# Optimization experiments

Measured on AMD Instinct MI355X. Metric: run time of the kernel, lower is better.

## Reference

```python
import jax, jax.numpy as jnp
import numpy as np

N = 50000
E = 800000
C = 96


def _mlp(x, W1, b1, W2, b2, out_act=None):
    # 2-layer MLP: Linear -> SiLU -> Linear -> (optional output activation)
    h = jax.nn.silu(x @ W1 + b1)
    y = h @ W2 + b2
    return y if out_act is None else out_act(y)


def setup_inputs() -> dict:
    key = jax.random.key(0)
    ks = jax.random.split(key, 16)
    s = 1.0 / np.sqrt(C)
    inp = {
        "node_feats": jax.random.normal(ks[0], (N, C), jnp.float32),
        "coordinates": jax.random.normal(ks[1], (N, 3), jnp.float32),
        "m_ji": jax.random.normal(ks[2], (E, C), jnp.float32),
        "edge_indices": jax.random.randint(ks[3], (2, E), 0, N, jnp.int64),
        # phi_n: 2C -> C -> C
        "Wn1": jax.random.normal(ks[4], (2 * C, C), jnp.float32) * s,
        "bn1": jnp.zeros((C,), jnp.float32),
        "Wn2": jax.random.normal(ks[5], (C, C), jnp.float32) * s,
        "bn2": jnp.zeros((C,), jnp.float32),
        # attention: C -> C -> 1, Sigmoid output
        "Wa1": jax.random.normal(ks[6], (C, C), jnp.float32) * s,
        "ba1": jnp.zeros((C,), jnp.float32),
        "Wa2": jax.random.normal(ks[7], (C, 1), jnp.float32) * s,
        "ba2": jnp.zeros((1,), jnp.float32),
        # phi_x: C -> C -> 1, no output activation
        "Wx1": jax.random.normal(ks[8], (C, C), jnp.float32) * s,
        "bx1": jnp.zeros((C,), jnp.float32),
        "Wx2": jax.random.normal(ks[9], (C, 1), jnp.float32) * s,
        "bx2": jnp.zeros((1,), jnp.float32),
    }
    return inp


def reference(node_feats, coordinates, m_ji, edge_indices,
              Wn1, bn1, Wn2, bn2, Wa1, ba1, Wa2, ba2, Wx1, bx1, Wx2, bx2):
    num_nodes = node_feats.shape[0]
    receiver = edge_indices[0]
    sender = edge_indices[1]

    # edge attention: [E, 1]
    attention_ji = _mlp(m_ji, Wa1, ba1, Wa2, ba2, out_act=jax.nn.sigmoid)

    # attention-weighted scatter-sum of messages into nodes: [N, C]
    m_i = jax.ops.segment_sum(m_ji * attention_ji, receiver, num_segments=num_nodes)

    # residual node update
    node_feats = _mlp(jnp.concatenate([node_feats, m_i], axis=-1), Wn1, bn1, Wn2, bn2) + node_feats

    # coordinate update (non-periodic: cell=None)
    r_ji = coordinates[sender] - coordinates[receiver]            # [E, 3]
    abs_r_ji = jnp.linalg.norm(r_ji, axis=-1, keepdims=True)       # [E, 1]
    delta_coords_ji = r_ji / (abs_r_ji + 1.0) * _mlp(m_ji, Wx1, bx1, Wx2, bx2)
    delta_coords_i = jax.ops.segment_sum(delta_coords_ji, receiver, num_segments=num_nodes)
    coordinates = coordinates + delta_coords_i

    return node_feats, coordinates, attention_ji
```

## Files before the change

### kernel.cpp

```cpp
#include <hip/hip_runtime.h>
#include <cstddef>

#define TC 96
#define BM 64
#define NT 256
#define AST 100
#define XST 204
#define HST 100

__device__ __forceinline__ float fsigmoid(float x) {
    return 1.0f / (1.0f + __expf(-x));
}

__global__ __launch_bounds__(NT, 4)
void edge_kernel(const float* __restrict__ m_ji,
                 const int*   __restrict__ edge_idx,
                 const float* __restrict__ coords,
                 const float* __restrict__ Wa1, const float* __restrict__ ba1,
                 const float* __restrict__ Wa2, const float* __restrict__ ba2,
                 const float* __restrict__ Wx1, const float* __restrict__ bx1,
                 const float* __restrict__ Wx2, const float* __restrict__ bx2,
                 float* __restrict__ m_acc,
                 float* __restrict__ out_coords,
                 float* __restrict__ out_att,
                 int E)
{
    __shared__ float A[BM][AST];
    __shared__ float s_att[BM];
    __shared__ float s_phx[BM];
    __shared__ int   s_recv[BM];
    __shared__ int   s_send[BM];

    const int tid  = threadIdx.x;
    const int e0   = blockIdx.x * BM;
    const int rows = (E - e0 < BM) ? (E - e0) : BM;

    if (tid < BM) {
        const int e = (tid < rows) ? (e0 + tid) : (E - 1);
        s_recv[tid] = edge_idx[e];
        s_send[tid] = edge_idx[E + e];
    }
    for (int i4 = tid; i4 < BM * (TC / 4); i4 += NT) {
        const int r  = i4 / (TC / 4);
        const int c4 = i4 % (TC / 4);
        const int er = (r < rows) ? (e0 + r) : (E - 1);
        const float4 v = *reinterpret_cast<const float4*>(m_ji + (size_t)er * TC + c4 * 4);
        *reinterpret_cast<float4*>(&A[r][c4 * 4]) = v;
    }
    __syncthreads();

    const int tx = tid & 15;
    const int ty = tid >> 4;
    const int r0 = ty * 4;
    const bool isAtt = (tx < 8);
    const float* __restrict__ Bp = isAtt ? (Wa1 + tx * 12) : (Wx1 + (tx - 8) * 12);

    float acc[4][12];
    #pragma unroll
    for (int q = 0; q < 4; ++q) {
        #pragma unroll
        for (int j = 0; j < 12; ++j) acc[q][j] = 0.0f;
    }

    #pragma unroll 2
    for (int k = 0; k < TC; ++k) {
        const float4 b0 = *reinterpret_cast<const float4*>(Bp + (size_t)k * TC + 0);
        const float4 b1 = *reinterpret_cast<const float4*>(Bp + (size_t)k * TC + 4);
        const float4 b2 = *reinterpret_cast<const float4*>(Bp + (size_t)k * TC + 8);
        const float bv[12] = {b0.x, b0.y, b0.z, b0.w,
                              b1.x, b1.y, b1.z, b1.w,
                              b2.x, b2.y, b2.z, b2.w};
        const float a0 = A[r0 + 0][k];
        const float a1 = A[r0 + 1][k];
        const float a2 = A[r0 + 2][k];
        const float a3 = A[r0 + 3][k];
        #pragma unroll
        for (int j = 0; j < 12; ++j) {
            acc[0][j] = fmaf(a0, bv[j], acc[0][j]);
            acc[1][j] = fmaf(a1, bv[j], acc[1][j]);
            acc[2][j] = fmaf(a2, bv[j], acc[2][j]);
            acc[3][j] = fmaf(a3, bv[j], acc[3][j]);
        }
    }

    const float* __restrict__ b1p = isAtt ? (ba1 + tx * 12) : (bx1 + (tx - 8) * 12);
    const float* __restrict__ w2p = isAtt ? (Wa2 + tx * 12) : (Wx2 + (tx - 8) * 12);
    float b1v[12], w2v[12];
    #pragma unroll
    for (int j = 0; j < 12; ++j) { b1v[j] = b1p[j]; w2v[j] = w2p[j]; }

    float red[4];
    #pragma unroll
    for (int q = 0; q < 4; ++q) {
        float p = 0.0f;
        #pragma unroll
        for (int j = 0; j < 12; ++j) {
            const float h = acc[q][j] + b1v[j];
            p = fmaf(h * fsigmoid(h), w2v[j], p);
        }
        red[q] = p;
    }
    #pragma unroll
    for (int m = 1; m <= 4; m <<= 1) {
        #pragma unroll
        for (int q = 0; q < 4; ++q) red[q] += __shfl_xor(red[q], m, 64);
    }
    if (tx == 0) {
        const float ba2v = ba2[0];
        #pragma unroll
        for (int q = 0; q < 4; ++q) s_att[r0 + q] = fsigmoid(red[q] + ba2v);
    }
    if (tx == 8) {
        const float bx2v = bx2[0];
        #pragma unroll
        for (int q = 0; q < 4; ++q) s_phx[r0 + q] = red[q] + bx2v;
    }
    __syncthreads();

    if (tid < rows) out_att[e0 + tid] = s_att[tid];

    for (int i = tid; i < rows * TC; i += NT) {
        const int r = i / TC;
        const int c = i - r * TC;
        atomicAdd(&m_acc[(size_t)s_recv[r] * TC + c], s_att[r] * A[r][c]);
    }

    if (tid < rows) {
        const int rcv = s_recv[tid];
        const int snd = s_send[tid];
        const float dx = coords[snd * 3 + 0] - coords[rcv * 3 + 0];
        const float dy = coords[snd * 3 + 1] - coords[rcv * 3 + 1];
        const float dz = coords[snd * 3 + 2] - coords[rcv * 3 + 2];
        const float nr = sqrtf(dx * dx + dy * dy + dz * dz);
        const float f  = s_phx[tid] / (nr + 1.0f);
        atomicAdd(&out_coords[rcv * 3 + 0], dx * f);
        atomicAdd(&out_coords[rcv * 3 + 1], dy * f);
        atomicAdd(&out_coords[rcv * 3 + 2], dz * f);
    }
}

__global__ __launch_bounds__(NT, 2)
void node_kernel(const float* __restrict__ node_feats,
                 const float* __restrict__ m_acc,
                 const float* __restrict__ Wn1, const float* __restrict__ bn1,
                 const float* __restrict__ Wn2, const float* __restrict__ bn2,
                 float* __restrict__ out_nf,
                 int N)
{
    __shared__ float X[BM][XST];
    __shared__ float H[BM][HST];

    const int tid = threadIdx.x;
    const int n0  = blockIdx.x * BM;

    for (int i4 = tid; i4 < BM * 48; i4 += NT) {
        const int r  = i4 / 48;
        const int c4 = i4 % 48;
        int node = n0 + r;
        if (node >= N) node = N - 1;
        float4 v;
        if (c4 < 24) v = *reinterpret_cast<const float4*>(node_feats + (size_t)node * TC + c4 * 4);
        else         v = *reinterpret_cast<const float4*>(m_acc + (size_t)node * TC + (c4 - 24) * 4);
        *reinterpret_cast<float4*>(&X[r][c4 * 4]) = v;
    }
    __syncthreads();

    const int tx = tid & 15;
    const int ty = tid >> 4;
    const int r0 = ty * 4;
    const int c0 = tx * 6;

    float acc[4][6];
    #pragma unroll
    for (int q = 0; q < 4; ++q) {
        #pragma unroll
        for (int j = 0; j < 6; ++j) acc[q][j] = 0.0f;
    }
    #pragma unroll 2
    for (int k = 0; k < 2 * TC; ++k) {
        const float2 b0 = *reinterpret_cast<const float2*>(Wn1 + (size_t)k * TC + c0 + 0);
        const float2 b1 = *reinterpret_cast<const float2*>(Wn1 + (size_t)k * TC + c0 + 2);
        const float2 b2 = *reinterpret_cast<const float2*>(Wn1 + (size_t)k * TC + c0 + 4);
        const float bv[6] = {b0.x, b0.y, b1.x, b1.y, b2.x, b2.y};
        const float a0 = X[r0 + 0][k];
        const float a1 = X[r0 + 1][k];
        const float a2 = X[r0 + 2][k];
        const float a3 = X[r0 + 3][k];
        #pragma unroll
        for (int j = 0; j < 6; ++j) {
            acc[0][j] = fmaf(a0, bv[j], acc[0][j]);
            acc[1][j] = fmaf(a1, bv[j], acc[1][j]);
            acc[2][j] = fmaf(a2, bv[j], acc[2][j]);
            acc[3][j] = fmaf(a3, bv[j], acc[3][j]);
        }
    }
    {
        float bnv[6];
        #pragma unroll
        for (int j = 0; j < 6; ++j) bnv[j] = bn1[c0 + j];
        #pragma unroll
        for (int q = 0; q < 4; ++q) {
            #pragma unroll
            for (int j = 0; j < 6; ++j) {
                const float h = acc[q][j] + bnv[j];
                H[r0 + q][c0 + j] = h * fsigmoid(h);
            }
        }
    }
    __syncthreads();

    float acc2[4][6];
    #pragma unroll
    for (int q = 0; q < 4; ++q) {
        #pragma unroll
        for (int j = 0; j < 6; ++j) acc2[q][j] = 0.0f;
    }
    #pragma unroll 2
    for (int k = 0; k < TC; ++k) {
        const float2 b0 = *reinterpret_cast<const float2*>(Wn2 + (size_t)k * TC + c0 + 0);
        const float2 b1 = *reinterpret_cast<const float2*>(Wn2 + (size_t)k * TC + c0 + 2);
        const float2 b2 = *reinterpret_cast<const float2*>(Wn2 + (size_t)k * TC + c0 + 4);
        const float bv[6] = {b0.x, b0.y, b1.x, b1.y, b2.x, b2.y};
        const float a0 = H[r0 + 0][k];
        const float a1 = H[r0 + 1][k];
        const float a2 = H[r0 + 2][k];
        const float a3 = H[r0 + 3][k];
        #pragma unroll
        for (int j = 0; j < 6; ++j) {
            acc2[0][j] = fmaf(a0, bv[j], acc2[0][j]);
            acc2[1][j] = fmaf(a1, bv[j], acc2[1][j]);
            acc2[2][j] = fmaf(a2, bv[j], acc2[2][j]);
            acc2[3][j] = fmaf(a3, bv[j], acc2[3][j]);
        }
    }
    {
        float bnv[6];
        #pragma unroll
        for (int j = 0; j < 6; ++j) bnv[j] = bn2[c0 + j];
        #pragma unroll
        for (int q = 0; q < 4; ++q) {
            const int node = n0 + r0 + q;
            if (node < N) {
                #pragma unroll
                for (int j = 0; j < 6; ++j) {
                    out_nf[(size_t)node * TC + c0 + j] = acc2[q][j] + bnv[j] + X[r0 + q][c0 + j];
                }
            }
        }
    }
}

extern "C" void kernel_launch(void* const* d_in, const int* in_sizes, int n_in,
                              void* d_out, int out_size, void* d_ws, size_t ws_size,
                              hipStream_t stream)
{
    const float* node_feats = (const float*)d_in[0];
    const float* coords     = (const float*)d_in[1];
    const float* m_ji       = (const float*)d_in[2];
    const int*   edge_idx   = (const int*)  d_in[3];
    const float* Wn1 = (const float*)d_in[4];
    const float* bn1 = (const float*)d_in[5];
    const float* Wn2 = (const float*)d_in[6];
    const float* bn2 = (const float*)d_in[7];
    const float* Wa1 = (const float*)d_in[8];
    const float* ba1 = (const float*)d_in[9];
    const float* Wa2 = (const float*)d_in[10];
    const float* ba2 = (const float*)d_in[11];
    const float* Wx1 = (const float*)d_in[12];
    const float* bx1 = (const float*)d_in[13];
    const float* Wx2 = (const float*)d_in[14];
    const float* bx2 = (const float*)d_in[15];

    const int N = in_sizes[0] / TC;
    const int E = in_sizes[2] / TC;

    float* out_nf     = (float*)d_out;
    float* out_coords = out_nf + (size_t)N * TC;
    float* out_att    = out_coords + (size_t)N * 3;
    float* m_acc      = (float*)d_ws;

    hipMemsetAsync(m_acc, 0, (size_t)N * TC * sizeof(float), stream);
    hipMemcpyAsync(out_coords, coords, (size_t)N * 3 * sizeof(float),
                   hipMemcpyDeviceToDevice, stream);

    const int edge_blocks = (E + BM - 1) / BM;
    edge_kernel<<<edge_blocks, NT, 0, stream>>>(
        m_ji, edge_idx, coords,
        Wa1, ba1, Wa2, ba2, Wx1, bx1, Wx2, bx2,
        m_acc, out_coords, out_att, E);

    const int node_blocks = (N + BM - 1) / BM;
    node_kernel<<<node_blocks, NT, 0, stream>>>(
        node_feats, m_acc, Wn1, bn1, Wn2, bn2, out_nf, N);
}
```

Baseline: 1.109 ms.

## Use split-bf16 MFMA for edge MLPs in persistent edge kernel

```diff
diff --git a/kernel.cpp b/kernel.cpp
--- a/kernel.cpp
+++ b/kernel.cpp
@@ -2,17 +2,23 @@
 #include <cstddef>
 
 #define TC 96
+#define NT 256
+#define EBM 128
+#define AST 104
+#define WST 196
 #define BM 64
-#define NT 256
-#define AST 100
 #define XST 204
 #define HST 100
+
+typedef __bf16 bf16x8 __attribute__((ext_vector_type(8)));
+typedef __bf16 bf16x4 __attribute__((ext_vector_type(4)));
+typedef float  f32x4  __attribute__((ext_vector_type(4)));
 
 __device__ __forceinline__ float fsigmoid(float x) {
     return 1.0f / (1.0f + __expf(-x));
 }
 
-__global__ __launch_bounds__(NT, 4)
+__global__ __launch_bounds__(NT, 2)
 void edge_kernel(const float* __restrict__ m_ji,
                  const int*   __restrict__ edge_idx,
                  const float* __restrict__ coords,
@@ -23,119 +29,181 @@
                  float* __restrict__ m_acc,
                  float* __restrict__ out_coords,
                  float* __restrict__ out_att,
-                 int E)
+                 int E, int ntiles)
 {
-    __shared__ float A[BM][AST];
-    __shared__ float s_att[BM];
-    __shared__ float s_phx[BM];
-    __shared__ int   s_recv[BM];
-    __shared__ int   s_send[BM];
+    __shared__ __align__(16) unsigned char s_buf[96 * WST * 4];
+    __shared__ float s_red[4][EBM];
+    __shared__ float s_att[EBM];
+    __shared__ float s_phx[EBM];
+    __shared__ int   s_recv[EBM];
+    __shared__ int   s_send[EBM];
+
+    float*  Wst = (float*)s_buf;
+    __bf16* Ahi = (__bf16*)s_buf;
+    __bf16* Alo = (__bf16*)(s_buf + EBM * AST * 2);
 
     const int tid  = threadIdx.x;
-    const int e0   = blockIdx.x * BM;
-    const int rows = (E - e0 < BM) ? (E - e0) : BM;
-
-    if (tid < BM) {
-        const int e = (tid < rows) ? (e0 + tid) : (E - 1);
-        s_recv[tid] = edge_idx[e];
-        s_send[tid] = edge_idx[E + e];
-    }
-    for (int i4 = tid; i4 < BM * (TC / 4); i4 += NT) {
-        const int r  = i4 / (TC / 4);
-        const int c4 = i4 % (TC / 4);
-        const int er = (r < rows) ? (e0 + r) : (E - 1);
-        const float4 v = *reinterpret_cast<const float4*>(m_ji + (size_t)er * TC + c4 * 4);
-        *reinterpret_cast<float4*>(&A[r][c4 * 4]) = v;
+    const int lane = tid & 63;
+    const int wave = tid >> 6;
+    const int lr   = lane & 15;
+    const int lq   = lane >> 4;
+
+    for (int i = tid; i < 96 * 48; i += NT) {
+        const int k  = i / 48;
+        const int c4 = i % 48;
+        const float* src = (c4 < 24) ? (Wa1 + (size_t)k * TC + c4 * 4)
+                                     : (Wx1 + (size_t)k * TC + (c4 - 24) * 4);
+        const float4 v = *reinterpret_cast<const float4*>(src);
+        *reinterpret_cast<float4*>(&Wst[k * WST + c4 * 4]) = v;
     }
     __syncthreads();
 
-    const int tx = tid & 15;
-    const int ty = tid >> 4;
-    const int r0 = ty * 4;
-    const bool isAtt = (tx < 8);
-    const float* __restrict__ Bp = isAtt ? (Wa1 + tx * 12) : (Wx1 + (tx - 8) * 12);
-
-    float acc[4][12];
+    bf16x8 BH[3][3], BL[3][3];
     #pragma unroll
-    for (int q = 0; q < 4; ++q) {
-        #pragma unroll
-        for (int j = 0; j < 12; ++j) acc[q][j] = 0.0f;
-    }
-
-    #pragma unroll 2
-    for (int k = 0; k < TC; ++k) {
-        const float4 b0 = *reinterpret_cast<const float4*>(Bp + (size_t)k * TC + 0);
-        const float4 b1 = *reinterpret_cast<const float4*>(Bp + (size_t)k * TC + 4);
-        const float4 b2 = *reinterpret_cast<const float4*>(Bp + (size_t)k * TC + 8);
-        const float bv[12] = {b0.x, b0.y, b0.z, b0.w,
-                              b1.x, b1.y, b1.z, b1.w,
-                              b2.x, b2.y, b2.z, b2.w};
-        const float a0 = A[r0 + 0][k];
-        const float a1 = A[r0 + 1][k];
-        const float a2 = A[r0 + 2][k];
-        const float a3 = A[r0 + 3][k];
-        #pragma unroll
-        for (int j = 0; j < 12; ++j) {
-            acc[0][j] = fmaf(a0, bv[j], acc[0][j]);
-            acc[1][j] = fmaf(a1, bv[j], acc[1][j]);
-            acc[2][j] = fmaf(a2, bv[j], acc[2][j]);
-            acc[3][j] = fmaf(a3, bv[j], acc[3][j]);
-        }
-    }
-
-    const float* __restrict__ b1p = isAtt ? (ba1 + tx * 12) : (bx1 + (tx - 8) * 12);
-    const float* __restrict__ w2p = isAtt ? (Wa2 + tx * 12) : (Wx2 + (tx - 8) * 12);
-    float b1v[12], w2v[12];
+    for (int nt = 0; nt < 3; ++nt) {
+        const int n = wave * 48 + nt * 16 + lr;
+        #pragma unroll
+        for (int c = 0; c < 3; ++c) {
+            #pragma unroll
+            for (int j = 0; j < 8; ++j) {
+                const int k = c * 32 + lq * 8 + j;
+                const float w = Wst[k * WST + n];
+                const __bf16 h = (__bf16)w;
+                BH[nt][c][j] = h;
+                BL[nt][c][j] = (__bf16)(w - (float)h);
+            }
+        }
+    }
+    const bool isAtt = (wave < 2);
+    const float* b1src = isAtt ? ba1 : bx1;
+    const float* w2src = isAtt ? Wa2 : Wx2;
+    float b1v[3], w2v[3];
     #pragma unroll
-    for (int j = 0; j < 12; ++j) { b1v[j] = b1p[j]; w2v[j] = w2p[j]; }
-
-    float red[4];
-    #pragma unroll
-    for (int q = 0; q < 4; ++q) {
-        float p = 0.0f;
-        #pragma unroll
-        for (int j = 0; j < 12; ++j) {
-            const float h = acc[q][j] + b1v[j];
-            p = fmaf(h * fsigmoid(h), w2v[j], p);
-        }
-        red[q] = p;
-    }
-    #pragma unroll
-    for (int m = 1; m <= 4; m <<= 1) {
-        #pragma unroll
-        for (int q = 0; q < 4; ++q) red[q] += __shfl_xor(red[q], m, 64);
-    }
-    if (tx == 0) {
-        const float ba2v = ba2[0];
-        #pragma unroll
-        for (int q = 0; q < 4; ++q) s_att[r0 + q] = fsigmoid(red[q] + ba2v);
-    }
-    if (tx == 8) {
-        const float bx2v = bx2[0];
-        #pragma unroll
-        for (int q = 0; q < 4; ++q) s_phx[r0 + q] = red[q] + bx2v;
-    }
-    __syncthreads();
-
-    if (tid < rows) out_att[e0 + tid] = s_att[tid];
-
-    for (int i = tid; i < rows * TC; i += NT) {
-        const int r = i / TC;
-        const int c = i - r * TC;
-        atomicAdd(&m_acc[(size_t)s_recv[r] * TC + c], s_att[r] * A[r][c]);
-    }
-
-    if (tid < rows) {
-        const int rcv = s_recv[tid];
-        const int snd = s_send[tid];
-        const float dx = coords[snd * 3 + 0] - coords[rcv * 3 + 0];
-        const float dy = coords[snd * 3 + 1] - coords[rcv * 3 + 1];
-        const float dz = coords[snd * 3 + 2] - coords[rcv * 3 + 2];
-        const float nr = sqrtf(dx * dx + dy * dy + dz * dz);
-        const float f  = s_phx[tid] / (nr + 1.0f);
-        atomicAdd(&out_coords[rcv * 3 + 0], dx * f);
-        atomicAdd(&out_coords[rcv * 3 + 1], dy * f);
-        atomicAdd(&out_coords[rcv * 3 + 2], dz * f);
+    for (int nt = 0; nt < 3; ++nt) {
+        const int nl = (wave & 1) * 48 + nt * 16 + lr;
+        b1v[nt] = b1src[nl];
+        w2v[nt] = w2src[nl];
+    }
+    const float ba2v = ba2[0];
+    const float bx2v = bx2[0];
+
+    for (int tile = blockIdx.x; tile < ntiles; tile += gridDim.x) {
+        const int e0   = tile * EBM;
+        const int rows = (E - e0 < EBM) ? (E - e0) : EBM;
+
+        __syncthreads();
+
+        if (tid < EBM) {
+            const int e = (tid < rows) ? (e0 + tid) : (E - 1);
+            s_recv[tid] = edge_idx[e];
+            s_send[tid] = edge_idx[E + e];
+        }
+        for (int i = tid; i < EBM * 24; i += NT) {
+            const int r  = i / 24;
+            const int c4 = i % 24;
+            const int e  = (r < rows) ? (e0 + r) : (E - 1);
+            const float4 v = *reinterpret_cast<const float4*>(&m_ji[(size_t)e * TC + c4 * 4]);
+            bf16x4 hv, lv;
+            const float vv[4] = {v.x, v.y, v.z, v.w};
+            #pragma unroll
+            for (int j = 0; j < 4; ++j) {
+                const __bf16 h = (__bf16)vv[j];
+                hv[j] = h;
+                lv[j] = (__bf16)(vv[j] - (float)h);
+            }
+            *reinterpret_cast<bf16x4*>(&Ahi[r * AST + c4 * 4]) = hv;
+            *reinterpret_cast<bf16x4*>(&Alo[r * AST + c4 * 4]) = lv;
+        }
+        __syncthreads();
+
+        #pragma unroll
+        for (int mp = 0; mp < 4; ++mp) {
+            f32x4 acc[2][3];
+            #pragma unroll
+            for (int s = 0; s < 2; ++s)
+                #pragma unroll
+                for (int nt = 0; nt < 3; ++nt)
+                    acc[s][nt] = (f32x4){0.f, 0.f, 0.f, 0.f};
+
+            #pragma unroll
+            for (int c = 0; c < 3; ++c) {
+                const int koff = c * 32 + lq * 8;
+                const int row0 = (mp * 2 + 0) * 16 + lr;
+                const int row1 = (mp * 2 + 1) * 16 + lr;
+                const bf16x8 aH0 = *reinterpret_cast<const bf16x8*>(&Ahi[row0 * AST + koff]);
+                const bf16x8 aL0 = *reinterpret_cast<const bf16x8*>(&Alo[row0 * AST + koff]);
+                const bf16x8 aH1 = *reinterpret_cast<const bf16x8*>(&Ahi[row1 * AST + koff]);
+                const bf16x8 aL1 = *reinterpret_cast<const bf16x8*>(&Alo[row1 * AST + koff]);
+                #pragma unroll
+                for (int nt = 0; nt < 3; ++nt) {
+                    acc[0][nt] = __builtin_amdgcn_mfma_f32_16x16x32_bf16(aH0, BH[nt][c], acc[0][nt], 0, 0, 0);
+                    acc[1][nt] = __builtin_amdgcn_mfma_f32_16x16x32_bf16(aH1, BH[nt][c], acc[1][nt], 0, 0, 0);
+                    acc[0][nt] = __builtin_amdgcn_mfma_f32_16x16x32_bf16(aL0, BH[nt][c], acc[0][nt], 0, 0, 0);
+                    acc[1][nt] = __builtin_amdgcn_mfma_f32_16x16x32_bf16(aL1, BH[nt][c], acc[1][nt], 0, 0, 0);
+                    acc[0][nt] = __builtin_amdgcn_mfma_f32_16x16x32_bf16(aH0, BL[nt][c], acc[0][nt], 0, 0, 0);
+                    acc[1][nt] = __builtin_amdgcn_mfma_f32_16x16x32_bf16(aH1, BL[nt][c], acc[1][nt], 0, 0, 0);
+                }
+            }
+
+            #pragma unroll
+            for (int s = 0; s < 2; ++s) {
+                float p[4] = {0.f, 0.f, 0.f, 0.f};
+                #pragma unroll
+                for (int nt = 0; nt < 3; ++nt) {
+                    #pragma unroll
+                    for (int q = 0; q < 4; ++q) {
+                        const float h = acc[s][nt][q] + b1v[nt];
+                        p[q] = fmaf(h * fsigmoid(h), w2v[nt], p[q]);
+                    }
+                }
+                #pragma unroll
+                for (int m = 1; m <= 8; m <<= 1) {
+                    #pragma unroll
+                    for (int q = 0; q < 4; ++q) p[q] += __shfl_xor(p[q], m, 64);
+                }
+                if (lr == 0) {
+                    const int rbase = (mp * 2 + s) * 16 + lq * 4;
+                    #pragma unroll
+                    for (int q = 0; q < 4; ++q) s_red[wave][rbase + q] = p[q];
+                }
+            }
+        }
+        __syncthreads();
+
+        if (tid < EBM) {
+            const float sa = s_red[0][tid] + s_red[1][tid] + ba2v;
+            const float sx = s_red[2][tid] + s_red[3][tid] + bx2v;
+            const float att = fsigmoid(sa);
+            s_att[tid] = att;
+            s_phx[tid] = sx;
+            if (tid < rows) out_att[e0 + tid] = att;
+        }
+        __syncthreads();
+
+        for (int i = tid; i < rows * 24; i += NT) {
+            const int r  = i / 24;
+            const int c4 = (i % 24) * 4;
+            const bf16x4 hv = *reinterpret_cast<const bf16x4*>(&Ahi[r * AST + c4]);
+            const bf16x4 lv = *reinterpret_cast<const bf16x4*>(&Alo[r * AST + c4]);
+            const float a = s_att[r];
+            float* dst = &m_acc[(size_t)s_recv[r] * TC + c4];
+            #pragma unroll
+            for (int j = 0; j < 4; ++j) {
+                atomicAdd(dst + j, a * ((float)hv[j] + (float)lv[j]));
+            }
+        }
+        if (tid < rows) {
+            const int rcv = s_recv[tid];
+            const int snd = s_send[tid];
+            const float dx = coords[snd * 3 + 0] - coords[rcv * 3 + 0];
+            const float dy = coords[snd * 3 + 1] - coords[rcv * 3 + 1];
+            const float dz = coords[snd * 3 + 2] - coords[rcv * 3 + 2];
+            const float nr = sqrtf(dx * dx + dy * dy + dz * dz);
+            const float f  = s_phx[tid] / (nr + 1.0f);
+            atomicAdd(&out_coords[rcv * 3 + 0], dx * f);
+            atomicAdd(&out_coords[rcv * 3 + 1], dy * f);
+            atomicAdd(&out_coords[rcv * 3 + 2], dz * f);
+        }
     }
 }
 
@@ -283,11 +351,12 @@
     hipMemcpyAsync(out_coords, coords, (size_t)N * 3 * sizeof(float),
                    hipMemcpyDeviceToDevice, stream);
 
-    const int edge_blocks = (E + BM - 1) / BM;
+    const int ntiles = (E + EBM - 1) / EBM;
+    const int edge_blocks = 512;
     edge_kernel<<<edge_blocks, NT, 0, stream>>>(
         m_ji, edge_idx, coords,
         Wa1, ba1, Wa2, ba2, Wx1, bx1, Wx2, bx2,
-        m_acc, out_coords, out_att, E);
+        m_acc, out_coords, out_att, E, ntiles);
 
     const int node_blocks = (N + BM - 1) / BM;
     node_kernel<<<node_blocks, NT, 0, stream>>>(
```

Result: slower. 1.615 ms (+45.6%).
